# Performance work log

Measured on AMD Instinct MI355X. Metric: run time of the kernel, lower is better.

The kernel has to match this reference:

```python
import jax, jax.numpy as jnp
import numpy as np
from math import sqrt

B, L, D, H = 2, 2048, 1024, 16
DH = D // H


def setup_inputs() -> dict:
    key = jax.random.key(0)
    ks = jax.random.split(key, 12)
    s = 1.0 / sqrt(D)
    inp = {
        'q': jax.random.normal(ks[0], (B, L, D), jnp.float32),
        'k': jax.random.normal(ks[1], (B, L, D), jnp.float32),
        'v': jax.random.normal(ks[2], (B, L, D), jnp.float32),
        'mask': jnp.zeros((B, 1, L, L), dtype=bool),
        'Wq': jax.random.normal(ks[3], (D, D), jnp.float32) * s,
        'bq': jnp.zeros((D,), jnp.float32),
        'Wk': jax.random.normal(ks[4], (D, D), jnp.float32) * s,
        'bk': jnp.zeros((D,), jnp.float32),
        'Wv': jax.random.normal(ks[5], (D, D), jnp.float32) * s,
        'bv': jnp.zeros((D,), jnp.float32),
        'Wo': jax.random.normal(ks[6], (D, D), jnp.float32) * s,
        'bo': jnp.zeros((D,), jnp.float32),
    }
    return inp


def _split(x):
    # [B, L, D] -> [B, H, L, DH]
    b, l, _ = x.shape
    return x.reshape(b, l, H, DH).transpose(0, 2, 1, 3)


def reference(q, k, v, mask, Wq, bq, Wk, bk, Wv, bv, Wo, bo):
    qh = _split(q @ Wq.T + bq)
    kh = _split(k @ Wk.T + bk)
    vh = _split(v @ Wv.T + bv)
    scores = jnp.einsum('bhqd,bhkd->bhqk', qh, kh) / sqrt(DH)
    scores = jnp.where(mask, -jnp.inf, scores)
    attn = jax.nn.softmax(scores, axis=-1)
    out = jnp.einsum('bhqk,bhkd->bhqd', attn, vh)
    out = out.transpose(0, 2, 1, 3).reshape(q.shape[0], -1, D)
    return out @ Wo.T + bo
```

## Files before the change

kernel.cpp:

```cpp
#include <hip/hip_runtime.h>
#include <hip/hip_bf16.h>
#include <stdint.h>

#define B_    2
#define L_    2048
#define D_    1024
#define H_    16
#define DH_   64
#define MTOT  (B_ * L_)

typedef __attribute__((ext_vector_type(8)))  short short8;
typedef __attribute__((ext_vector_type(4)))  float f32x4;
typedef __attribute__((ext_vector_type(16))) float f32x16;
typedef __attribute__((ext_vector_type(4)))  unsigned int u32x4;

static __device__ __forceinline__ short f2bf(float f) {
    uint32_t u = __builtin_bit_cast(uint32_t, f);
    uint32_t r = (u + 0x7fffu + ((u >> 16) & 1u)) >> 16;
    return (short)r;
}

static __device__ __forceinline__ void load_lds16(const short* g, short* l) {
    __builtin_amdgcn_global_load_lds(
        (const __attribute__((address_space(1))) unsigned int*)g,
        (__attribute__((address_space(3))) unsigned int*)l,
        16, 0, 0);
}

__global__ __launch_bounds__(256) void cvt_all(
        const float* __restrict__ s0, const float* __restrict__ s1,
        const float* __restrict__ s2, const float* __restrict__ s3,
        const float* __restrict__ s4, const float* __restrict__ s5,
        const float* __restrict__ s6,
        short* __restrict__ d0, short* __restrict__ d1, short* __restrict__ d2,
        short* __restrict__ d3, short* __restrict__ d4, short* __restrict__ d5,
        short* __restrict__ d6) {
    const int y = blockIdx.y;
    if (y >= 3 && blockIdx.x >= 512) return;
    const float* s; short* d;
    switch (y) {
        case 0: s = s0; d = d0; break;
        case 1: s = s1; d = d1; break;
        case 2: s = s2; d = d2; break;
        case 3: s = s3; d = d3; break;
        case 4: s = s4; d = d4; break;
        case 5: s = s5; d = d5; break;
        default: s = s6; d = d6; break;
    }
    size_t i = ((size_t)blockIdx.x * 256 + threadIdx.x) * 8;
    float4 x = *(const float4*)(s + i);
    float4 yv = *(const float4*)(s + i + 4);
    short8 o;
    o[0] = f2bf(x.x); o[1] = f2bf(x.y); o[2] = f2bf(x.z); o[3] = f2bf(x.w);
    o[4] = f2bf(yv.x); o[5] = f2bf(yv.y); o[6] = f2bf(yv.z); o[7] = f2bf(yv.w);
    *(short8*)(d + i) = o;
}

template <typename OutT>
static __device__ __forceinline__ void gemm_bt_body(
        const short* __restrict__ A, const short* __restrict__ W,
        const float* __restrict__ bias, OutT* __restrict__ C, float oscale) {
    constexpr int K = 1024, N = 1024;
    __shared__ short As[128 * 32];
    __shared__ short Ws[128 * 32];
    const int tid  = threadIdx.x;
    const int wid  = tid >> 6;
    const int lane = tid & 63;
    const int wr = wid >> 1, wc = wid & 1;
    const int g = lane >> 4, r = lane & 15;
    const int rowbase = blockIdx.y * 128;
    const int colbase = blockIdx.x * 128;

    f32x4 acc[4][4] = {};

    for (int k0 = 0; k0 < K; k0 += 32) {
#pragma unroll
        for (int i = 0; i < 2; i++) {
            int c   = i * 256 + wid * 64 + lane;
            int row = c >> 2;
            int col = (c & 3) * 8;
            load_lds16(A + (size_t)(rowbase + row) * K + k0 + col,
                       As + (size_t)(i * 256 + wid * 64) * 8);
            load_lds16(W + (size_t)(colbase + row) * K + k0 + col,
                       Ws + (size_t)(i * 256 + wid * 64) * 8);
        }
        __syncthreads();

        short8 af[4], bf[4];
#pragma unroll
        for (int mi = 0; mi < 4; mi++)
            af[mi] = *(const short8*)&As[(wr * 64 + mi * 16 + r) * 32 + g * 8];
#pragma unroll
        for (int ni = 0; ni < 4; ni++)
            bf[ni] = *(const short8*)&Ws[(wc * 64 + ni * 16 + r) * 32 + g * 8];
#pragma unroll
        for (int mi = 0; mi < 4; mi++)
#pragma unroll
            for (int ni = 0; ni < 4; ni++)
                acc[mi][ni] = __builtin_amdgcn_mfma_f32_16x16x32_bf16(
                    af[mi], bf[ni], acc[mi][ni], 0, 0, 0);
        __syncthreads();
    }

#pragma unroll
    for (int mi = 0; mi < 4; mi++)
#pragma unroll
        for (int ni = 0; ni < 4; ni++) {
            int row0 = rowbase + wr * 64 + mi * 16 + g * 4;
            int col  = colbase + wc * 64 + ni * 16 + r;
            float bb = bias[col];
#pragma unroll
            for (int t = 0; t < 4; t++) {
                float val = (acc[mi][ni][t] + bb) * oscale;
                size_t idx = (size_t)(row0 + t) * N + col;
                if constexpr (__is_same(OutT, short)) C[idx] = f2bf(val);
                else                                  C[idx] = val;
            }
        }
}

__global__ __launch_bounds__(256) void gemm_proj3(
        const short* __restrict__ Qa, const short* __restrict__ Ka, const short* __restrict__ Va,
        const short* __restrict__ Wq, const short* __restrict__ Wk, const short* __restrict__ Wv,
        const float* __restrict__ bq, const float* __restrict__ bk, const float* __restrict__ bv,
        short* __restrict__ Qo, short* __restrict__ Ko, short* __restrict__ Vo, float qscale) {
    const short* A; const short* W; const float* bias; short* C; float sc;
    if (blockIdx.z == 0)      { A = Qa; W = Wq; bias = bq; C = Qo; sc = qscale; }
    else if (blockIdx.z == 1) { A = Ka; W = Wk; bias = bk; C = Ko; sc = 1.0f; }
    else                      { A = Va; W = Wv; bias = bv; C = Vo; sc = 1.0f; }
    gemm_bt_body<short>(A, W, bias, C, sc);
}

__global__ __launch_bounds__(256) void gemm_out(
        const short* __restrict__ A, const short* __restrict__ W,
        const float* __restrict__ bias, float* __restrict__ C) {
    gemm_bt_body<float>(A, W, bias, C, 1.0f);
}

__global__ __launch_bounds__(512, 4) void attn_kernel(
        const short* __restrict__ Qp, const short* __restrict__ Kp,
        const short* __restrict__ Vp, short* __restrict__ Ao) {
    const int bh = blockIdx.y;
    const int b  = bh >> 4;
    const int h  = bh & 15;
    const int q0 = blockIdx.x * 128;
    const int tid = threadIdx.x;
    const int w   = tid >> 6;
    const int l   = tid & 63;
    const int l31 = l & 31;
    const int hi  = l >> 5;
    const int kg  = w >> 2;
    const int qw  = w & 3;
    const size_t rowbase = (size_t)b * L_;
    const int kbase = kg * (L_ / 2);

    __shared__ short KS[2][2][64 * 64];
    __shared__ short VT[2][2][64 * 64];

    const int qrow = q0 + qw * 32 + l31;
    short8 qf[4];
    {
        const short* qptr = Qp + (rowbase + qrow) * D_ + h * 64 + hi * 8;
#pragma unroll
        for (int s16 = 0; s16 < 4; s16++)
            qf[s16] = *(const short8*)(qptr + s16 * 16);
    }

    f32x16 o0 = {0.f,0.f,0.f,0.f,0.f,0.f,0.f,0.f,0.f,0.f,0.f,0.f,0.f,0.f,0.f,0.f};
    f32x16 o1 = o0;
    float lpart = 0.f;

    const int rsw = l31 & 7;
    int qkoff[4];
#pragma unroll
    for (int s16 = 0; s16 < 4; s16++)
        qkoff[s16] = ((s16 * 2 + hi) ^ rsw) << 4;
    const int rowb0 = l31 * 128;
    const int rowb1 = (32 + l31) * 128;
    const int vsw = ((l31 & 7) << 4) ^ (((l31 >> 3) & 3) << 5);
    int voff[2][2];
#pragma unroll
    for (int ks = 0; ks < 2; ks++)
#pragma unroll
        for (int kk = 0; kk < 2; kk++)
            voff[ks][kk] = (ks * 64 + kk * 32 + hi * 16) ^ vsw;

    const short* kbase_p = Kp + (rowbase + kbase + qw * 8 + (l >> 3)) * D_ +
                           h * 64 + (((l & 7) ^ ((l >> 3) & 7)) * 8);
    auto stageK = [&](int buf, int t) {
        const short* src = kbase_p + (size_t)t * 64 * D_;
        short* dst = &KS[kg][buf][qw * 512];
        load_lds16(src, dst);
        load_lds16(src + (size_t)32 * D_, dst + 2048);
    };

    const int gt = tid & 255;
    const int pr = gt >> 3;
    const int c0 = gt & 7;
    const int spr = (pr & 0x19) | ((pr & 2) << 1) | ((pr & 4) >> 1);
    const int svbase = (spr * 4) ^ ((c0 & 3) << 5);
    const short* vptr = Vp + (rowbase + kbase + 2 * pr) * D_ + h * 64 + c0 * 8;

    short8 vr0, vr1;
    auto loadV = [&](int t) {
        const size_t off = (size_t)t * 64 * D_;
        vr0 = *(const short8*)(vptr + off);
        vr1 = *(const short8*)(vptr + off + D_);
    };
    auto writeVt = [&](int buf) {
        char* Vt = (char*)&VT[kg][buf][0];
        u32x4 w0 = __builtin_bit_cast(u32x4, vr0);
        u32x4 w1 = __builtin_bit_cast(u32x4, vr1);
#pragma unroll
        for (int jj = 0; jj < 8; jj++) {
            uint32_t pk = __builtin_amdgcn_perm(
                w0[jj >> 1], w1[jj >> 1],
                (jj & 1) ? 0x03020706u : 0x01000504u);
            *(uint32_t*)(Vt + c0 * 1024 + jj * 128 + (svbase ^ (jj << 4))) = pk;
        }
    };

    auto qk = [&](const char* ksb, int ks) -> f32x16 {
        f32x16 s = {0.f,0.f,0.f,0.f,0.f,0.f,0.f,0.f,0.f,0.f,0.f,0.f,0.f,0.f,0.f,0.f};
        const char* kb = ksb + ks * 4096 + rowb0;
        __builtin_amdgcn_s_setprio(1);
#pragma unroll
        for (int s16 = 0; s16 < 4; s16++) {
            short8 kf = *(const short8*)(kb + qkoff[s16]);
            s = __builtin_amdgcn_mfma_f32_32x32x16_bf16(kf, qf[s16], s, 0, 0, 0);
        }
        __builtin_amdgcn_s_setprio(0);
        return s;
    };

    auto smpv = [&](f32x16 s, int ks, const char* vtb) {
#pragma unroll
        for (int i = 0; i < 16; i++) s[i] = __builtin_amdgcn_exp2f(s[i]);
        {
            float t0 = (s[0] + s[1]) + (s[2] + s[3]);
            float t1 = (s[4] + s[5]) + (s[6] + s[7]);
            float t2 = (s[8] + s[9]) + (s[10] + s[11]);
            float t3 = (s[12] + s[13]) + (s[14] + s[15]);
            lpart += (t0 + t1) + (t2 + t3);
        }
        uint32_t wd[8];
#pragma unroll
        for (int i = 0; i < 8; i++)
            asm("v_cvt_pk_bf16_f32 %0, %1, %2"
                : "=v"(wd[i]) : "v"(s[2 * i]), "v"(s[2 * i + 1]));
        u32x4 a0 = { wd[0], wd[1], wd[2], wd[3] };
        u32x4 a1 = { wd[4], wd[5], wd[6], wd[7] };
        short8 pf0 = __builtin_bit_cast(short8, a0);
        short8 pf1 = __builtin_bit_cast(short8, a1);
        __builtin_amdgcn_s_setprio(1);
#pragma unroll
        for (int kk = 0; kk < 2; kk++) {
            short8 pf = (kk == 0) ? pf0 : pf1;
            short8 vf0 = *(const short8*)(vtb + rowb0 + voff[ks][kk]);
            o0 = __builtin_amdgcn_mfma_f32_32x32x16_bf16(pf, vf0, o0, 0, 0, 0);
            short8 vf1 = *(const short8*)(vtb + rowb1 + voff[ks][kk]);
            o1 = __builtin_amdgcn_mfma_f32_32x32x16_bf16(pf, vf1, o1, 0, 0, 0);
        }
        __builtin_amdgcn_s_setprio(0);
    };

    stageK(0, 0);
    loadV(0);
    writeVt(0);
    __syncthreads();

    constexpr int NT = (L_ / 2) / 64;
    for (int t = 0; t < NT; t++) {
        const int cur = t & 1, nxt = cur ^ 1;
        const bool pre = (t + 1 < NT);
        if (pre) {
            stageK(nxt, t + 1);
            loadV(t + 1);
        }
        const char* ksb = (const char*)&KS[kg][cur][0];
        const char* vtb = (const char*)&VT[kg][cur][0];
        f32x16 sA = qk(ksb, 0);
        f32x16 sB = qk(ksb, 1);
        smpv(sA, 0, vtb);
        smpv(sB, 1, vtb);
        if (pre) writeVt(nxt);
        __syncthreads();
    }

    float lrow = lpart + __shfl_xor(lpart, 32, 64);

    float* mrgO = (float*)&KS[0][0][0];
    float* mrgL = (float*)&VT[0][0][0];
    const int idx = qw * 64 + l;
    if (kg == 1) {
#pragma unroll
        for (int i = 0; i < 16; i++) {
            mrgO[i * 256 + idx]        = o0[i];
            mrgO[(16 + i) * 256 + idx] = o1[i];
        }
        mrgL[idx] = lrow;
    }
    __syncthreads();
    if (kg == 0) {
        float lsum = lrow + mrgL[idx];
#pragma unroll
        for (int rr = 0; rr < 16; rr++) {
            int crow  = (rr & 3) + 8 * (rr >> 2) + 4 * hi;
            float lq  = __shfl(lsum, crow, 64);
            float inv = 1.0f / lq;
            float v0 = (o0[rr] + mrgO[rr * 256 + idx])        * inv;
            float v1 = (o1[rr] + mrgO[(16 + rr) * 256 + idx]) * inv;
            int row = q0 + qw * 32 + crow;
            size_t base = (rowbase + row) * D_ + h * 64 + l31;
            Ao[base]      = f2bf(v0);
            Ao[base + 32] = f2bf(v1);
        }
    }
}

extern "C" void kernel_launch(void* const* d_in, const int* in_sizes, int n_in,
                              void* d_out, int out_size, void* d_ws, size_t ws_size,
                              hipStream_t stream) {
    const float* q  = (const float*)d_in[0];
    const float* k  = (const float*)d_in[1];
    const float* v  = (const float*)d_in[2];
    const float* Wq = (const float*)d_in[4];
    const float* bq = (const float*)d_in[5];
    const float* Wk = (const float*)d_in[6];
    const float* bk = (const float*)d_in[7];
    const float* Wv = (const float*)d_in[8];
    const float* bv = (const float*)d_in[9];
    const float* Wo = (const float*)d_in[10];
    const float* bo = (const float*)d_in[11];
    float* out = (float*)d_out;

    char* ws = (char*)d_ws;
    const size_t SZ_ACT = (size_t)MTOT * D_ * sizeof(short);
    const size_t SZ_W   = (size_t)D_ * D_ * sizeof(short);
    short* Qb  = (short*)(ws);
    short* Kb  = (short*)(ws + SZ_ACT);
    short* Vb  = (short*)(ws + 2 * SZ_ACT);
    short* Wqb = (short*)(ws + 3 * SZ_ACT);
    short* Wkb = (short*)(ws + 3 * SZ_ACT + SZ_W);
    short* Wvb = (short*)(ws + 3 * SZ_ACT + 2 * SZ_W);
    short* Wob = (short*)(ws + 3 * SZ_ACT + 3 * SZ_W);
    short* Qp  = (short*)(ws + 3 * SZ_ACT + 4 * SZ_W);
    short* Kp  = (short*)(ws + 4 * SZ_ACT + 4 * SZ_W);
    short* Vp  = (short*)(ws + 5 * SZ_ACT + 4 * SZ_W);
    short* Ao  = Qb;

    const float qscale = 0.125f * 1.4426950408889634f;

    cvt_all<<<dim3(2048, 7, 1), 256, 0, stream>>>(
        q, k, v, Wq, Wk, Wv, Wo, Qb, Kb, Vb, Wqb, Wkb, Wvb, Wob);
    gemm_proj3<<<dim3(8, 32, 3), 256, 0, stream>>>(Qb, Kb, Vb, Wqb, Wkb, Wvb,
                                                   bq, bk, bv, Qp, Kp, Vp, qscale);
    attn_kernel<<<dim3(16, 32, 1), 512, 0, stream>>>(Qp, Kp, Vp, Ao);
    gemm_out<<<dim3(8, 32, 1), 256, 0, stream>>>(Ao, Wob, bo, out);
}
```

Baseline: 133.6 us.

## Write V projection pre-transposed and swizzled, stage it with async LDS loads

The V projection GEMM epilogue now writes V transposed per head (d-major over keys) in the pre-swizzled order the attention kernel expects. The attention kernel can then stage V tiles with direct global-to-LDS loads, like K, instead of register loads followed by permute-and-scatter LDS writes each iteration. This takes VALU and LDS write work out of the attention inner loop. In exchange, the GEMM epilogue for V does scattered 8-byte stores, which may coalesce less well.

```diff
diff --git a/kernel.cpp b/kernel.cpp
--- a/kernel.cpp
+++ b/kernel.cpp
@@ -12,6 +12,7 @@
 typedef __attribute__((ext_vector_type(8)))  short short8;
 typedef __attribute__((ext_vector_type(4)))  float f32x4;
 typedef __attribute__((ext_vector_type(16))) float f32x16;
+typedef __attribute__((ext_vector_type(2)))  unsigned int u32x2;
 typedef __attribute__((ext_vector_type(4)))  unsigned int u32x4;
 
 static __device__ __forceinline__ short f2bf(float f) {
@@ -56,10 +57,10 @@
     *(short8*)(d + i) = o;
 }
 
-template <typename OutT>
+template <int MODE>
 static __device__ __forceinline__ void gemm_bt_body(
         const short* __restrict__ A, const short* __restrict__ W,
-        const float* __restrict__ bias, OutT* __restrict__ C, float oscale) {
+        const float* __restrict__ bias, void* __restrict__ Cv, float oscale) {
     constexpr int K = 1024, N = 1024;
     __shared__ short As[128 * 32];
     __shared__ short Ws[128 * 32];
@@ -109,12 +110,33 @@
             int row0 = rowbase + wr * 64 + mi * 16 + g * 4;
             int col  = colbase + wc * 64 + ni * 16 + r;
             float bb = bias[col];
-#pragma unroll
-            for (int t = 0; t < 4; t++) {
-                float val = (acc[mi][ni][t] + bb) * oscale;
-                size_t idx = (size_t)(row0 + t) * N + col;
-                if constexpr (__is_same(OutT, short)) C[idx] = f2bf(val);
-                else                                  C[idx] = val;
+            float v0 = (acc[mi][ni][0] + bb) * oscale;
+            float v1 = (acc[mi][ni][1] + bb) * oscale;
+            float v2 = (acc[mi][ni][2] + bb) * oscale;
+            float v3 = (acc[mi][ni][3] + bb) * oscale;
+            if constexpr (MODE == 2) {
+                int bb_ = row0 >> 11;
+                int kk  = row0 & 2047;
+                int hh  = col >> 6, dd = col & 63;
+                int c0  = (kk >> 1) & 31;
+                int sc0 = (c0 & 0x19) | ((c0 & 2) << 1) | ((c0 & 4) >> 1);
+                size_t base = ((size_t)((bb_ * 16 + hh) * 64 + dd)) * 2048 +
+                              (size_t)(kk >> 6) * 64 + sc0 * 2;
+                uint32_t w0 = (uint32_t)(uint16_t)f2bf(v0) |
+                              ((uint32_t)(uint16_t)f2bf(v1) << 16);
+                uint32_t w1 = (uint32_t)(uint16_t)f2bf(v2) |
+                              ((uint32_t)(uint16_t)f2bf(v3) << 16);
+                u32x2 pk = { w0, w1 };
+                *(u32x2*)((short*)Cv + base) = pk;
+            } else if constexpr (MODE == 1) {
+                float* C = (float*)Cv;
+                size_t idx = (size_t)row0 * N + col;
+                C[idx] = v0; C[idx + N] = v1; C[idx + 2 * N] = v2; C[idx + 3 * N] = v3;
+            } else {
+                short* C = (short*)Cv;
+                size_t idx = (size_t)row0 * N + col;
+                C[idx] = f2bf(v0); C[idx + N] = f2bf(v1);
+                C[idx + 2 * N] = f2bf(v2); C[idx + 3 * N] = f2bf(v3);
             }
         }
 }
@@ -123,23 +145,21 @@
         const short* __restrict__ Qa, const short* __restrict__ Ka, const short* __restrict__ Va,
         const short* __restrict__ Wq, const short* __restrict__ Wk, const short* __restrict__ Wv,
         const float* __restrict__ bq, const float* __restrict__ bk, const float* __restrict__ bv,
-        short* __restrict__ Qo, short* __restrict__ Ko, short* __restrict__ Vo, float qscale) {
-    const short* A; const short* W; const float* bias; short* C; float sc;
-    if (blockIdx.z == 0)      { A = Qa; W = Wq; bias = bq; C = Qo; sc = qscale; }
-    else if (blockIdx.z == 1) { A = Ka; W = Wk; bias = bk; C = Ko; sc = 1.0f; }
-    else                      { A = Va; W = Wv; bias = bv; C = Vo; sc = 1.0f; }
-    gemm_bt_body<short>(A, W, bias, C, sc);
+        short* __restrict__ Qo, short* __restrict__ Ko, short* __restrict__ VtG, float qscale) {
+    if (blockIdx.z == 0)      gemm_bt_body<0>(Qa, Wq, bq, Qo, qscale);
+    else if (blockIdx.z == 1) gemm_bt_body<0>(Ka, Wk, bk, Ko, 1.0f);
+    else                      gemm_bt_body<2>(Va, Wv, bv, VtG, 1.0f);
 }
 
 __global__ __launch_bounds__(256) void gemm_out(
         const short* __restrict__ A, const short* __restrict__ W,
         const float* __restrict__ bias, float* __restrict__ C) {
-    gemm_bt_body<float>(A, W, bias, C, 1.0f);
+    gemm_bt_body<1>(A, W, bias, C, 1.0f);
 }
 
 __global__ __launch_bounds__(512, 4) void attn_kernel(
         const short* __restrict__ Qp, const short* __restrict__ Kp,
-        const short* __restrict__ Vp, short* __restrict__ Ao) {
+        const short* __restrict__ VtG, short* __restrict__ Ao) {
     const int bh = blockIdx.y;
     const int b  = bh >> 4;
     const int h  = bh & 15;
@@ -194,30 +214,15 @@
         load_lds16(src + (size_t)32 * D_, dst + 2048);
     };
 
-    const int gt = tid & 255;
-    const int pr = gt >> 3;
-    const int c0 = gt & 7;
-    const int spr = (pr & 0x19) | ((pr & 2) << 1) | ((pr & 4) >> 1);
-    const int svbase = (spr * 4) ^ ((c0 & 3) << 5);
-    const short* vptr = Vp + (rowbase + kbase + 2 * pr) * D_ + h * 64 + c0 * 8;
-
-    short8 vr0, vr1;
-    auto loadV = [&](int t) {
-        const size_t off = (size_t)t * 64 * D_;
-        vr0 = *(const short8*)(vptr + off);
-        vr1 = *(const short8*)(vptr + off + D_);
-    };
-    auto writeVt = [&](int buf) {
-        char* Vt = (char*)&VT[kg][buf][0];
-        u32x4 w0 = __builtin_bit_cast(u32x4, vr0);
-        u32x4 w1 = __builtin_bit_cast(u32x4, vr1);
-#pragma unroll
-        for (int jj = 0; jj < 8; jj++) {
-            uint32_t pk = __builtin_amdgcn_perm(
-                w0[jj >> 1], w1[jj >> 1],
-                (jj & 1) ? 0x03020706u : 0x01000504u);
-            *(uint32_t*)(Vt + c0 * 1024 + jj * 128 + (svbase ^ (jj << 4))) = pk;
-        }
+    const int vd = qw * 8 + (l >> 3);
+    const int vslot = (l & 7) ^ ((vd & 7) ^ (((vd >> 3) & 3) << 1));
+    const short* vbase_p = VtG + ((size_t)(bh * 64 + vd)) * 2048 +
+                           (size_t)kbase + vslot * 8;
+    auto stageV = [&](int buf, int t) {
+        const short* src = vbase_p + t * 64;
+        short* dst = &VT[kg][buf][qw * 512];
+        load_lds16(src, dst);
+        load_lds16(src + (size_t)32 * 2048, dst + 2048);
     };
 
     auto qk = [&](const char* ksb, int ks) -> f32x16 {
@@ -265,8 +270,7 @@
     };
 
     stageK(0, 0);
-    loadV(0);
-    writeVt(0);
+    stageV(0, 0);
     __syncthreads();
 
     constexpr int NT = (L_ / 2) / 64;
@@ -275,7 +279,7 @@
         const bool pre = (t + 1 < NT);
         if (pre) {
             stageK(nxt, t + 1);
-            loadV(t + 1);
+            stageV(nxt, t + 1);
         }
         const char* ksb = (const char*)&KS[kg][cur][0];
         const char* vtb = (const char*)&VT[kg][cur][0];
@@ -283,7 +287,6 @@
         f32x16 sB = qk(ksb, 1);
         smpv(sA, 0, vtb);
         smpv(sB, 1, vtb);
-        if (pre) writeVt(nxt);
         __syncthreads();
     }
 
@@ -346,7 +349,7 @@
     short* Wob = (short*)(ws + 3 * SZ_ACT + 3 * SZ_W);
     short* Qp  = (short*)(ws + 3 * SZ_ACT + 4 * SZ_W);
     short* Kp  = (short*)(ws + 4 * SZ_ACT + 4 * SZ_W);
-    short* Vp  = (short*)(ws + 5 * SZ_ACT + 4 * SZ_W);
+    short* VtG = (short*)(ws + 5 * SZ_ACT + 4 * SZ_W);
     short* Ao  = Qb;
 
     const float qscale = 0.125f * 1.4426950408889634f;
@@ -354,7 +357,7 @@
     cvt_all<<<dim3(2048, 7, 1), 256, 0, stream>>>(
         q, k, v, Wq, Wk, Wv, Wo, Qb, Kb, Vb, Wqb, Wkb, Wvb, Wob);
     gemm_proj3<<<dim3(8, 32, 3), 256, 0, stream>>>(Qb, Kb, Vb, Wqb, Wkb, Wvb,
-                                                   bq, bk, bv, Qp, Kp, Vp, qscale);
-    attn_kernel<<<dim3(16, 32, 1), 512, 0, stream>>>(Qp, Kp, Vp, Ao);
+                                                   bq, bk, bv, Qp, Kp, VtG, qscale);
+    attn_kernel<<<dim3(16, 32, 1), 512, 0, stream>>>(Qp, Kp, VtG, Ao);
     gemm_out<<<dim3(8, 32, 1), 256, 0, stream>>>(Ao, Wob, bo, out);
 }
```

Measured after the change: 143.9 us. 1.08x slower.

## Double-buffer LDS in projection GEMM and swizzle block order for L2 reuse

Applied to the files above, without the earlier changes.

The projection GEMM now keeps two LDS buffers per operand and issues the async global-to-LDS loads for the next k-step before the MFMAs on the current one, so memory latency can overlap with compute. It also remaps block indices so that consecutive blocks share row and column tiles, aiming for better L2 reuse. This doubles LDS use per block, which may lower occupancy, and it assumes a fixed 8x32 grid shape.

```diff
diff --git a/kernel.cpp b/kernel.cpp
--- a/kernel.cpp
+++ b/kernel.cpp
@@ -61,38 +61,51 @@
         const short* __restrict__ A, const short* __restrict__ W,
         const float* __restrict__ bias, OutT* __restrict__ C, float oscale) {
     constexpr int K = 1024, N = 1024;
-    __shared__ short As[128 * 32];
-    __shared__ short Ws[128 * 32];
+    __shared__ short As[2][128 * 32];
+    __shared__ short Ws[2][128 * 32];
     const int tid  = threadIdx.x;
     const int wid  = tid >> 6;
     const int lane = tid & 63;
     const int wr = wid >> 1, wc = wid & 1;
     const int g = lane >> 4, r = lane & 15;
-    const int rowbase = blockIdx.y * 128;
-    const int colbase = blockIdx.x * 128;
+
+    const int hid = blockIdx.y * 8 + blockIdx.x;
+    const int bid = (hid & 7) * 32 + (hid >> 3);
+    const int rowbase = (bid >> 3) * 128;
+    const int colbase = (bid & 7) * 128;
+
+    const int c0   = wid * 64 + lane;
+    const int srow = c0 >> 2;
+    const int scol = (c0 & 3) * 8;
+    const short* Abase = A + (size_t)(rowbase + srow) * K + scol;
+    const short* Wbase = W + (size_t)(colbase + srow) * K + scol;
+
+    auto stage = [&](int buf, int k0) {
+#pragma unroll
+        for (int i = 0; i < 2; i++) {
+            load_lds16(Abase + (size_t)i * 64 * K + k0,
+                       &As[buf][(i * 256 + wid * 64) * 8]);
+            load_lds16(Wbase + (size_t)i * 64 * K + k0,
+                       &Ws[buf][(i * 256 + wid * 64) * 8]);
+        }
+    };
 
     f32x4 acc[4][4] = {};
 
+    stage(0, 0);
+    __syncthreads();
+
     for (int k0 = 0; k0 < K; k0 += 32) {
-#pragma unroll
-        for (int i = 0; i < 2; i++) {
-            int c   = i * 256 + wid * 64 + lane;
-            int row = c >> 2;
-            int col = (c & 3) * 8;
-            load_lds16(A + (size_t)(rowbase + row) * K + k0 + col,
-                       As + (size_t)(i * 256 + wid * 64) * 8);
-            load_lds16(W + (size_t)(colbase + row) * K + k0 + col,
-                       Ws + (size_t)(i * 256 + wid * 64) * 8);
-        }
-        __syncthreads();
+        const int cur = (k0 >> 5) & 1, nxt = cur ^ 1;
+        if (k0 + 32 < K) stage(nxt, k0 + 32);
 
         short8 af[4], bf[4];
 #pragma unroll
         for (int mi = 0; mi < 4; mi++)
-            af[mi] = *(const short8*)&As[(wr * 64 + mi * 16 + r) * 32 + g * 8];
+            af[mi] = *(const short8*)&As[cur][(wr * 64 + mi * 16 + r) * 32 + g * 8];
 #pragma unroll
         for (int ni = 0; ni < 4; ni++)
-            bf[ni] = *(const short8*)&Ws[(wc * 64 + ni * 16 + r) * 32 + g * 8];
+            bf[ni] = *(const short8*)&Ws[cur][(wc * 64 + ni * 16 + r) * 32 + g * 8];
 #pragma unroll
         for (int mi = 0; mi < 4; mi++)
 #pragma unroll
```

Result: faster. 128.3 us (-4.0%).
